# Optimization experiments

Hardware: AMD Instinct MI355X
Metric: run time of the kernel (lower is better)

Reference implementation:

```python
import jax, jax.numpy as jnp
import numpy as np

N_NODES = 100000
N_EDGES = 1600000
N_PAIRS = 500000
NFEAT = 128
NHID = 128


def _uniform(key, shape, stdv):
    return jax.random.uniform(key, shape, jnp.float32, -stdv, stdv)


def setup_inputs() -> dict:
    key = jax.random.key(0)
    ks = jax.random.split(key, 24)
    inp = {
        'x': jax.random.normal(ks[0], (N_NODES, NFEAT), jnp.float32),
        'edge_row': jax.random.randint(ks[1], (N_EDGES,), 0, N_NODES, jnp.int32),
        'edge_col': jax.random.randint(ks[2], (N_EDGES,), 0, N_NODES, jnp.int32),
        'edge_w': jax.random.uniform(ks[3], (N_EDGES,), jnp.float32),
        'x_idx': jax.random.randint(ks[4], (N_PAIRS,), 0, N_NODES, jnp.int32),
        'y_idx': jax.random.randint(ks[5], (N_PAIRS,), 0, N_NODES, jnp.int32),
    }
    stdv = 1.0 / np.sqrt(NHID)
    # GCN layers: (weight_self, weight_neighbor, bias)
    inp['gc1_ws'] = _uniform(ks[6], (NFEAT, NHID), stdv)
    inp['gc1_wn'] = _uniform(ks[7], (NFEAT, NHID), stdv)
    inp['gc1_b'] = _uniform(ks[8], (NHID,), stdv)
    inp['gc2_ws'] = _uniform(ks[9], (NHID, NHID), stdv)
    inp['gc2_wn'] = _uniform(ks[10], (NHID, NHID), stdv)
    inp['gc2_b'] = _uniform(ks[11], (NHID,), stdv)
    inp['gc3_ws'] = _uniform(ks[12], (NHID, NHID), stdv)
    inp['gc3_wn'] = _uniform(ks[13], (NHID, NHID), stdv)
    inp['gc3_b'] = _uniform(ks[14], (NHID,), stdv)
    # MLP decoder: fc1 (2*nhid -> nhid), fc2 (nhid -> 1)
    s1 = 1.0 / np.sqrt(2 * NHID)
    inp['dec_w1'] = _uniform(ks[15], (2 * NHID, NHID), s1)
    inp['dec_b1'] = _uniform(ks[16], (NHID,), s1)
    s2 = 1.0 / np.sqrt(NHID)
    inp['dec_w2'] = _uniform(ks[17], (NHID, 1), s2)
    inp['dec_b2'] = _uniform(ks[18], (1,), s2)
    return inp


def _gcn(h, ws, wn, b, row, col, w, n_nodes):
    # act_self = h @ W_self ; act_neighbor = adj @ (h @ W_neighbor)
    act_self = h @ ws
    support = h @ wn  # [N, out]
    act_nb = jax.ops.segment_sum(support[col] * w[:, None], row,
                                 num_segments=n_nodes)
    return act_self + act_nb + b


def reference(x, edge_row, edge_col, edge_w, x_idx, y_idx,
              gc1_ws, gc1_wn, gc1_b, gc2_ws, gc2_wn, gc2_b,
              gc3_ws, gc3_wn, gc3_b, dec_w1, dec_b1, dec_w2, dec_b2):
    n = x.shape[0]
    h = jax.nn.relu(_gcn(x, gc1_ws, gc1_wn, gc1_b, edge_row, edge_col, edge_w, n))
    h = jax.nn.relu(_gcn(h, gc2_ws, gc2_wn, gc2_b, edge_row, edge_col, edge_w, n))
    z = _gcn(h, gc3_ws, gc3_wn, gc3_b, edge_row, edge_col, edge_w, n)
    # edge MLP decoder on gathered node pairs
    pair = jnp.concatenate([z[x_idx], z[y_idx]], axis=1)  # [P, 2*nhid]
    hdec = jax.nn.relu(pair @ dec_w1 + dec_b1)
    p = jax.nn.sigmoid(hdec @ dec_w2 + dec_b2)  # [P, 1]
    return (p, z)
```

## Files before the change

kernel.cpp:

```cpp
#include <hip/hip_runtime.h>
#include <hip/hip_bf16.h>

#define N_NODES 100000
#define N_EDGES 1600000
#define N_PAIRS 500000
#define MPAD    100032
#define NF      128

typedef __bf16 bf16x8 __attribute__((ext_vector_type(8)));
typedef float  f32x4  __attribute__((ext_vector_type(4)));
typedef unsigned int   u32;
typedef unsigned short u16;

__device__ inline u16   f2b(float f) { __bf16 b = (__bf16)f; return __builtin_bit_cast(u16, b); }
__device__ inline float b2f(u16 u)   { return (float)__builtin_bit_cast(__bf16, u); }

__global__ void k_convT(const float* __restrict__ src, u16* __restrict__ dst, int K, int N) {
    int i = blockIdx.x * 256 + threadIdx.x;
    if (i >= K * N) return;
    int n = i / K, k = i - n * K;
    dst[i] = f2b(src[k * N + n]);
}

__global__ void k_convX(const float2* __restrict__ x, u32* __restrict__ xb) {
    int i = blockIdx.x * 256 + threadIdx.x;
    if (i >= MPAD * 64) return;
    int node = i >> 6;
    float2 v = make_float2(0.f, 0.f);
    if (node < N_NODES) v = x[i];
    xb[i] = (u32)f2b(v.x) | ((u32)f2b(v.y) << 16);
}

__global__ void k_hist(const int* __restrict__ row, int* __restrict__ deg) {
    int e = blockIdx.x * 256 + threadIdx.x;
    if (e >= N_EDGES) return;
    atomicAdd(&deg[row[e]], 1);
}

__global__ void k_scan1(const int* __restrict__ deg, int* __restrict__ incl, int* __restrict__ bsums) {
    __shared__ int s[1024];
    int t = threadIdx.x;
    int g = blockIdx.x * 1024 + t;
    s[t] = (g < N_NODES) ? deg[g] : 0;
    __syncthreads();
    for (int d = 1; d < 1024; d <<= 1) {
        int add = (t >= d) ? s[t - d] : 0;
        __syncthreads();
        s[t] += add;
        __syncthreads();
    }
    if (g < N_NODES) incl[g] = s[t];
    if (t == 1023) bsums[blockIdx.x] = s[1023];
}

__global__ void k_scan2(int* __restrict__ bsums, int nb) {
    __shared__ int s[128];
    int t = threadIdx.x;
    s[t] = (t < nb) ? bsums[t] : 0;
    __syncthreads();
    for (int d = 1; d < 128; d <<= 1) {
        int add = (t >= d) ? s[t - d] : 0;
        __syncthreads();
        s[t] += add;
        __syncthreads();
    }
    if (t < nb) bsums[t] = (t == 0) ? 0 : s[t - 1];
}

__global__ void k_scan3(const int* __restrict__ incl, const int* __restrict__ bsums,
                        int* __restrict__ rowptr, int* __restrict__ cursor) {
    int g = blockIdx.x * 256 + threadIdx.x;
    if (g == 0) { rowptr[0] = 0; cursor[0] = 0; }
    if (g >= N_NODES) return;
    int v = incl[g] + bsums[g >> 10];
    rowptr[g + 1] = v;
    if (g + 1 < N_NODES) cursor[g + 1] = v;
}

__global__ void k_scatter(const int* __restrict__ row, const int* __restrict__ col,
                          const float* __restrict__ w, int* __restrict__ cursor,
                          int* __restrict__ ccol, float* __restrict__ cw) {
    int e = blockIdx.x * 256 + threadIdx.x;
    if (e >= N_EDGES) return;
    int pos = atomicAdd(&cursor[row[e]], 1);
    ccol[pos] = col[e];
    cw[pos]   = w[e];
}

__global__ void k_gemm_pair(const u16* __restrict__ A, const u16* __restrict__ WsT,
                            const u16* __restrict__ WnT, float* __restrict__ HS,
                            u16* __restrict__ SUPc) {
    int wid = threadIdx.x >> 6, lane = threadIdx.x & 63;
    int lr = lane & 15, lg = lane >> 4;
    int m0 = blockIdx.x * 64;
    const u16* WT = (wid < 2) ? WsT : WnT;
    int n0 = (wid & 1) * 64;
    f32x4 acc[4][4] = {};
    for (int ks = 0; ks < 4; ++ks) {
        int k0 = ks * 32 + lg * 8;
        bf16x8 a[4], b[4];
        #pragma unroll
        for (int r = 0; r < 4; ++r)
            a[r] = *reinterpret_cast<const bf16x8*>(A + (size_t)(m0 + r * 16 + lr) * NF + k0);
        #pragma unroll
        for (int c = 0; c < 4; ++c)
            b[c] = *reinterpret_cast<const bf16x8*>(WT + (size_t)(n0 + c * 16 + lr) * NF + k0);
        #pragma unroll
        for (int r = 0; r < 4; ++r)
            #pragma unroll
            for (int c = 0; c < 4; ++c)
                acc[r][c] = __builtin_amdgcn_mfma_f32_16x16x32_bf16(a[r], b[c], acc[r][c], 0, 0, 0);
    }
    #pragma unroll
    for (int r = 0; r < 4; ++r) {
        #pragma unroll
        for (int reg = 0; reg < 4; ++reg) {
            int m = m0 + r * 16 + lg * 4 + reg;
            if (m >= N_NODES) continue;
            #pragma unroll
            for (int c = 0; c < 4; ++c) {
                int col = n0 + c * 16 + lr;
                float v = acc[r][c][reg];
                if (wid < 2) HS[(size_t)m * NF + col] = v;
                else {
                    int ch = col >> 4, cc = col & 15;
                    SUPc[((size_t)ch * MPAD + m) * 16 + cc] = f2b(v);
                }
            }
        }
    }
}

__global__ void k_gemm_uv(const u16* __restrict__ A, const u16* __restrict__ W1aT,
                          const u16* __restrict__ W1bT, const float* __restrict__ b1,
                          u16* __restrict__ U, u16* __restrict__ V) {
    int wid = threadIdx.x >> 6, lane = threadIdx.x & 63;
    int lr = lane & 15, lg = lane >> 4;
    int m0 = blockIdx.x * 64;
    const u16* WT = (wid < 2) ? W1aT : W1bT;
    u16* OUT = (wid < 2) ? U : V;
    int addb = (wid < 2) ? 1 : 0;
    int n0 = (wid & 1) * 64;
    f32x4 acc[4][4] = {};
    for (int ks = 0; ks < 4; ++ks) {
        int k0 = ks * 32 + lg * 8;
        bf16x8 a[4], b[4];
        #pragma unroll
        for (int r = 0; r < 4; ++r)
            a[r] = *reinterpret_cast<const bf16x8*>(A + (size_t)(m0 + r * 16 + lr) * NF + k0);
        #pragma unroll
        for (int c = 0; c < 4; ++c)
            b[c] = *reinterpret_cast<const bf16x8*>(WT + (size_t)(n0 + c * 16 + lr) * NF + k0);
        #pragma unroll
        for (int r = 0; r < 4; ++r)
            #pragma unroll
            for (int c = 0; c < 4; ++c)
                acc[r][c] = __builtin_amdgcn_mfma_f32_16x16x32_bf16(a[r], b[c], acc[r][c], 0, 0, 0);
    }
    #pragma unroll
    for (int r = 0; r < 4; ++r) {
        #pragma unroll
        for (int reg = 0; reg < 4; ++reg) {
            int m = m0 + r * 16 + lg * 4 + reg;
            #pragma unroll
            for (int c = 0; c < 4; ++c) {
                int col = n0 + c * 16 + lr;
                float v = acc[r][c][reg];
                if (addb) v += b1[col];
                OUT[(size_t)m * NF + col] = f2b(v);
            }
        }
    }
}

__global__ void k_aggregate_c(const u32* __restrict__ SUPc, const float2* __restrict__ HS2,
                              const int* __restrict__ rowptr, const int* __restrict__ ccol,
                              const float* __restrict__ cw, const float2* __restrict__ bias2,
                              u32* __restrict__ Hout, float2* __restrict__ Zout, int relu) {
    int chunk = blockIdx.x & 7;
    int nb = blockIdx.x >> 3;
    int l = threadIdx.x & 63, w = threadIdx.x >> 6;
    int sub = l >> 3, sl = l & 7;
    int node = nb * 32 + w * 8 + sub;
    if (node >= N_NODES) return;
    const u32* base = SUPc + (size_t)chunk * MPAD * 8;
    int e0 = rowptr[node], e1 = rowptr[node + 1];
    float a0 = 0.f, a1 = 0.f;
    int e = e0;
    for (; e + 4 <= e1; e += 4) {
        int c0 = ccol[e], c1 = ccol[e + 1], c2 = ccol[e + 2], c3 = ccol[e + 3];
        float w0 = cw[e], w1 = cw[e + 1], w2 = cw[e + 2], w3 = cw[e + 3];
        u32 v0 = base[(size_t)c0 * 8 + sl];
        u32 v1 = base[(size_t)c1 * 8 + sl];
        u32 v2 = base[(size_t)c2 * 8 + sl];
        u32 v3 = base[(size_t)c3 * 8 + sl];
        a0 = fmaf(w0, b2f((u16)(v0 & 0xffff)), a0); a1 = fmaf(w0, b2f((u16)(v0 >> 16)), a1);
        a0 = fmaf(w1, b2f((u16)(v1 & 0xffff)), a0); a1 = fmaf(w1, b2f((u16)(v1 >> 16)), a1);
        a0 = fmaf(w2, b2f((u16)(v2 & 0xffff)), a0); a1 = fmaf(w2, b2f((u16)(v2 >> 16)), a1);
        a0 = fmaf(w3, b2f((u16)(v3 & 0xffff)), a0); a1 = fmaf(w3, b2f((u16)(v3 >> 16)), a1);
    }
    for (; e < e1; ++e) {
        int c = ccol[e];
        float wgt = cw[e];
        u32 v = base[(size_t)c * 8 + sl];
        a0 = fmaf(wgt, b2f((u16)(v & 0xffff)), a0);
        a1 = fmaf(wgt, b2f((u16)(v >> 16)), a1);
    }
    size_t oidx = (size_t)node * 64 + chunk * 8 + sl;
    float2 hsv = HS2[oidx];
    float2 bv  = bias2[chunk * 8 + sl];
    float o0 = hsv.x + a0 + bv.x;
    float o1 = hsv.y + a1 + bv.y;
    if (relu) { o0 = fmaxf(o0, 0.f); o1 = fmaxf(o1, 0.f); }
    Hout[oidx] = (u32)f2b(o0) | ((u32)f2b(o1) << 16);
    if (Zout) Zout[oidx] = make_float2(o0, o1);
}

__global__ void k_pairdec(const u16* __restrict__ U, const u16* __restrict__ V,
                          const int* __restrict__ xidx, const int* __restrict__ yidx,
                          const float* __restrict__ w2, const float* __restrict__ b2,
                          float* __restrict__ outp) {
    int t = blockIdx.x * 256 + threadIdx.x;
    int pair = t >> 2;
    int j = t & 3;
    if (pair >= N_PAIRS) return;
    int xi = xidx[pair], yi = yidx[pair];
    const bf16x8* up = reinterpret_cast<const bf16x8*>(U + (size_t)xi * NF + j * 32);
    const bf16x8* vp = reinterpret_cast<const bf16x8*>(V + (size_t)yi * NF + j * 32);
    bf16x8 uu[4], vv[4];
    #pragma unroll
    for (int it = 0; it < 4; ++it) { uu[it] = up[it]; vv[it] = vp[it]; }
    const float4* w4 = reinterpret_cast<const float4*>(w2 + j * 32);
    float acc = 0.f;
    #pragma unroll
    for (int it = 0; it < 4; ++it) {
        float4 wa = w4[it * 2], wb = w4[it * 2 + 1];
        float h;
        h = fmaxf((float)uu[it][0] + (float)vv[it][0], 0.f); acc = fmaf(h, wa.x, acc);
        h = fmaxf((float)uu[it][1] + (float)vv[it][1], 0.f); acc = fmaf(h, wa.y, acc);
        h = fmaxf((float)uu[it][2] + (float)vv[it][2], 0.f); acc = fmaf(h, wa.z, acc);
        h = fmaxf((float)uu[it][3] + (float)vv[it][3], 0.f); acc = fmaf(h, wa.w, acc);
        h = fmaxf((float)uu[it][4] + (float)vv[it][4], 0.f); acc = fmaf(h, wb.x, acc);
        h = fmaxf((float)uu[it][5] + (float)vv[it][5], 0.f); acc = fmaf(h, wb.y, acc);
        h = fmaxf((float)uu[it][6] + (float)vv[it][6], 0.f); acc = fmaf(h, wb.z, acc);
        h = fmaxf((float)uu[it][7] + (float)vv[it][7], 0.f); acc = fmaf(h, wb.w, acc);
    }
    acc += __shfl_xor(acc, 1, 64);
    acc += __shfl_xor(acc, 2, 64);
    if (j == 0) outp[pair] = 1.f / (1.f + __expf(-(acc + b2[0])));
}

extern "C" void kernel_launch(void* const* d_in, const int* in_sizes, int n_in,
                              void* d_out, int out_size, void* d_ws, size_t ws_size,
                              hipStream_t stream) {
    const float* x      = (const float*)d_in[0];
    const int* edge_row = (const int*)d_in[1];
    const int* edge_col = (const int*)d_in[2];
    const float* edge_w = (const float*)d_in[3];
    const int* x_idx    = (const int*)d_in[4];
    const int* y_idx    = (const int*)d_in[5];
    const float* gws[3] = {(const float*)d_in[6], (const float*)d_in[9],  (const float*)d_in[12]};
    const float* gwn[3] = {(const float*)d_in[7], (const float*)d_in[10], (const float*)d_in[13]};
    const float* gb[3]  = {(const float*)d_in[8], (const float*)d_in[11], (const float*)d_in[14]};
    const float* dw1 = (const float*)d_in[15];
    const float* db1 = (const float*)d_in[16];
    const float* dw2 = (const float*)d_in[17];
    const float* db2 = (const float*)d_in[18];
    float* out_p = (float*)d_out;
    float* out_z = out_p + N_PAIRS;

    char* base = (char*)d_ws;
    size_t off = 0;
    auto alloc = [&](size_t bytes) -> void* {
        void* p = base + off;
        off = (off + bytes + 255) & ~(size_t)255;
        return p;
    };
    u16* h0   = (u16*)alloc((size_t)MPAD * NF * 2);
    u16* h1   = (u16*)alloc((size_t)MPAD * NF * 2);
    u16* supc = (u16*)alloc((size_t)MPAD * NF * 2);
    float* hs = (float*)alloc((size_t)MPAD * NF * 4);
    u16* wT[6];
    for (int i = 0; i < 6; ++i) wT[i] = (u16*)alloc(128 * 128 * 2);
    u16* w1aT = (u16*)alloc(128 * 128 * 2);
    u16* w1bT = (u16*)alloc(128 * 128 * 2);
    int* deg    = (int*)alloc(N_NODES * 4);
    int* incl   = (int*)alloc(N_NODES * 4);
    int* bsums  = (int*)alloc(128 * 4);
    int* rowptr = (int*)alloc((N_NODES + 1) * 4);
    int* cursor = (int*)alloc(N_NODES * 4);
    int* ccol   = (int*)alloc(N_EDGES * 4);
    float* cwt  = (float*)alloc(N_EDGES * 4);
    u16* U = (u16*)hs;
    u16* V = U + (size_t)MPAD * NF;

    hipMemsetAsync(deg, 0, N_NODES * 4, stream);

    for (int l = 0; l < 3; ++l) {
        k_convT<<<64, 256, 0, stream>>>(gws[l], wT[2 * l],     128, 128);
        k_convT<<<64, 256, 0, stream>>>(gwn[l], wT[2 * l + 1], 128, 128);
    }
    k_convT<<<64, 256, 0, stream>>>(dw1,             w1aT, 128, 128);
    k_convT<<<64, 256, 0, stream>>>(dw1 + 128 * 128, w1bT, 128, 128);
    k_convX<<<(MPAD * 64 + 255) / 256, 256, 0, stream>>>((const float2*)x, (u32*)h0);

    k_hist<<<(N_EDGES + 255) / 256, 256, 0, stream>>>(edge_row, deg);
    k_scan1<<<98, 1024, 0, stream>>>(deg, incl, bsums);
    k_scan2<<<1, 128, 0, stream>>>(bsums, 98);
    k_scan3<<<(N_NODES + 255) / 256, 256, 0, stream>>>(incl, bsums, rowptr, cursor);
    k_scatter<<<(N_EDGES + 255) / 256, 256, 0, stream>>>(edge_row, edge_col, edge_w, cursor, ccol, cwt);

    const int GB = MPAD / 64;
    const int AB = 8 * ((N_NODES + 31) / 32);

    k_gemm_pair<<<GB, 256, 0, stream>>>(h0, wT[0], wT[1], hs, supc);
    k_aggregate_c<<<AB, 256, 0, stream>>>((const u32*)supc, (const float2*)hs, rowptr, ccol, cwt,
                                          (const float2*)gb[0], (u32*)h1, nullptr, 1);
    k_gemm_pair<<<GB, 256, 0, stream>>>(h1, wT[2], wT[3], hs, supc);
    k_aggregate_c<<<AB, 256, 0, stream>>>((const u32*)supc, (const float2*)hs, rowptr, ccol, cwt,
                                          (const float2*)gb[1], (u32*)h0, nullptr, 1);
    k_gemm_pair<<<GB, 256, 0, stream>>>(h0, wT[4], wT[5], hs, supc);
    k_aggregate_c<<<AB, 256, 0, stream>>>((const u32*)supc, (const float2*)hs, rowptr, ccol, cwt,
                                          (const float2*)gb[2], (u32*)h1, (float2*)out_z, 0);
    k_gemm_uv<<<GB, 256, 0, stream>>>(h1, w1aT, w1bT, db1, U, V);
    k_pairdec<<<(N_PAIRS * 4 + 255) / 256, 256, 0, stream>>>(U, V, x_idx, y_idx, dw2, db2, out_p);
}
```

Measured before the change: 905.0 us.

## Pack CSR col/weight into u64, store self-activation in bf16, add nontemporal hints

The CSR column index and edge weight are packed into a single 64-bit entry, so the aggregation fetches one 8-byte value per edge instead of two separate 4-byte arrays, and the edge loop is unrolled to 8 to keep more gathers in flight. The self-term output of the paired GEMM is now stored as bf16 instead of fp32, halving its write and read traffic. Nontemporal loads and stores are added on streaming accesses to reduce cache pollution. Keeping the self-term in bf16 adds rounding error to the output z.

```diff
diff --git a/kernel.cpp b/kernel.cpp
--- a/kernel.cpp
+++ b/kernel.cpp
@@ -9,8 +9,10 @@
 
 typedef __bf16 bf16x8 __attribute__((ext_vector_type(8)));
 typedef float  f32x4  __attribute__((ext_vector_type(4)));
-typedef unsigned int   u32;
-typedef unsigned short u16;
+typedef float  f32x2  __attribute__((ext_vector_type(2)));
+typedef unsigned int       u32;
+typedef unsigned short     u16;
+typedef unsigned long long u64;
 
 __device__ inline u16   f2b(float f) { __bf16 b = (__bf16)f; return __builtin_bit_cast(u16, b); }
 __device__ inline float b2f(u16 u)   { return (float)__builtin_bit_cast(__bf16, u); }
@@ -22,12 +24,12 @@
     dst[i] = f2b(src[k * N + n]);
 }
 
-__global__ void k_convX(const float2* __restrict__ x, u32* __restrict__ xb) {
+__global__ void k_convX(const f32x2* __restrict__ x, u32* __restrict__ xb) {
     int i = blockIdx.x * 256 + threadIdx.x;
     if (i >= MPAD * 64) return;
     int node = i >> 6;
-    float2 v = make_float2(0.f, 0.f);
-    if (node < N_NODES) v = x[i];
+    f32x2 v = {0.f, 0.f};
+    if (node < N_NODES) v = __builtin_nontemporal_load(x + i);
     xb[i] = (u32)f2b(v.x) | ((u32)f2b(v.y) << 16);
 }
 
@@ -79,16 +81,18 @@
 
 __global__ void k_scatter(const int* __restrict__ row, const int* __restrict__ col,
                           const float* __restrict__ w, int* __restrict__ cursor,
-                          int* __restrict__ ccol, float* __restrict__ cw) {
+                          u64* __restrict__ cce) {
     int e = blockIdx.x * 256 + threadIdx.x;
     if (e >= N_EDGES) return;
-    int pos = atomicAdd(&cursor[row[e]], 1);
-    ccol[pos] = col[e];
-    cw[pos]   = w[e];
+    int r = __builtin_nontemporal_load(row + e);
+    int c = __builtin_nontemporal_load(col + e);
+    float wv = __builtin_nontemporal_load(w + e);
+    int pos = atomicAdd(&cursor[r], 1);
+    cce[pos] = ((u64)__builtin_bit_cast(u32, wv) << 32) | (u32)c;
 }
 
 __global__ void k_gemm_pair(const u16* __restrict__ A, const u16* __restrict__ WsT,
-                            const u16* __restrict__ WnT, float* __restrict__ HS,
+                            const u16* __restrict__ WnT, u16* __restrict__ HSb,
                             u16* __restrict__ SUPc) {
     int wid = threadIdx.x >> 6, lane = threadIdx.x & 63;
     int lr = lane & 15, lg = lane >> 4;
@@ -120,11 +124,11 @@
             #pragma unroll
             for (int c = 0; c < 4; ++c) {
                 int col = n0 + c * 16 + lr;
-                float v = acc[r][c][reg];
-                if (wid < 2) HS[(size_t)m * NF + col] = v;
+                u16 v = f2b(acc[r][c][reg]);
+                if (wid < 2) __builtin_nontemporal_store(v, HSb + (size_t)m * NF + col);
                 else {
                     int ch = col >> 4, cc = col & 15;
-                    SUPc[((size_t)ch * MPAD + m) * 16 + cc] = f2b(v);
+                    SUPc[((size_t)ch * MPAD + m) * 16 + cc] = v;
                 }
             }
         }
@@ -173,10 +177,10 @@
     }
 }
 
-__global__ void k_aggregate_c(const u32* __restrict__ SUPc, const float2* __restrict__ HS2,
-                              const int* __restrict__ rowptr, const int* __restrict__ ccol,
-                              const float* __restrict__ cw, const float2* __restrict__ bias2,
-                              u32* __restrict__ Hout, float2* __restrict__ Zout, int relu) {
+__global__ void k_aggregate_c(const u32* __restrict__ SUPc, const u32* __restrict__ HSb,
+                              const int* __restrict__ rowptr, const u64* __restrict__ cce,
+                              const f32x2* __restrict__ bias2,
+                              u32* __restrict__ Hout, f32x2* __restrict__ Zout, int relu) {
     int chunk = blockIdx.x & 7;
     int nb = blockIdx.x >> 3;
     int l = threadIdx.x & 63, w = threadIdx.x >> 6;
@@ -187,33 +191,38 @@
     int e0 = rowptr[node], e1 = rowptr[node + 1];
     float a0 = 0.f, a1 = 0.f;
     int e = e0;
-    for (; e + 4 <= e1; e += 4) {
-        int c0 = ccol[e], c1 = ccol[e + 1], c2 = ccol[e + 2], c3 = ccol[e + 3];
-        float w0 = cw[e], w1 = cw[e + 1], w2 = cw[e + 2], w3 = cw[e + 3];
-        u32 v0 = base[(size_t)c0 * 8 + sl];
-        u32 v1 = base[(size_t)c1 * 8 + sl];
-        u32 v2 = base[(size_t)c2 * 8 + sl];
-        u32 v3 = base[(size_t)c3 * 8 + sl];
-        a0 = fmaf(w0, b2f((u16)(v0 & 0xffff)), a0); a1 = fmaf(w0, b2f((u16)(v0 >> 16)), a1);
-        a0 = fmaf(w1, b2f((u16)(v1 & 0xffff)), a0); a1 = fmaf(w1, b2f((u16)(v1 >> 16)), a1);
-        a0 = fmaf(w2, b2f((u16)(v2 & 0xffff)), a0); a1 = fmaf(w2, b2f((u16)(v2 >> 16)), a1);
-        a0 = fmaf(w3, b2f((u16)(v3 & 0xffff)), a0); a1 = fmaf(w3, b2f((u16)(v3 >> 16)), a1);
+    for (; e + 8 <= e1; e += 8) {
+        u64 r[8];
+        u32 v[8];
+        #pragma unroll
+        for (int i = 0; i < 8; ++i) r[i] = __builtin_nontemporal_load(cce + e + i);
+        #pragma unroll
+        for (int i = 0; i < 8; ++i) v[i] = base[(size_t)(u32)r[i] * 8 + sl];
+        #pragma unroll
+        for (int i = 0; i < 8; ++i) {
+            float wt = __builtin_bit_cast(float, (u32)(r[i] >> 32));
+            a0 = fmaf(wt, b2f((u16)(v[i] & 0xffff)), a0);
+            a1 = fmaf(wt, b2f((u16)(v[i] >> 16)), a1);
+        }
     }
     for (; e < e1; ++e) {
-        int c = ccol[e];
-        float wgt = cw[e];
-        u32 v = base[(size_t)c * 8 + sl];
-        a0 = fmaf(wgt, b2f((u16)(v & 0xffff)), a0);
-        a1 = fmaf(wgt, b2f((u16)(v >> 16)), a1);
+        u64 rr = __builtin_nontemporal_load(cce + e);
+        u32 v = base[(size_t)(u32)rr * 8 + sl];
+        float wt = __builtin_bit_cast(float, (u32)(rr >> 32));
+        a0 = fmaf(wt, b2f((u16)(v & 0xffff)), a0);
+        a1 = fmaf(wt, b2f((u16)(v >> 16)), a1);
     }
     size_t oidx = (size_t)node * 64 + chunk * 8 + sl;
-    float2 hsv = HS2[oidx];
-    float2 bv  = bias2[chunk * 8 + sl];
-    float o0 = hsv.x + a0 + bv.x;
-    float o1 = hsv.y + a1 + bv.y;
+    u32 hsv = __builtin_nontemporal_load(HSb + oidx);
+    f32x2 bv = bias2[chunk * 8 + sl];
+    float o0 = b2f((u16)(hsv & 0xffff)) + a0 + bv.x;
+    float o1 = b2f((u16)(hsv >> 16)) + a1 + bv.y;
     if (relu) { o0 = fmaxf(o0, 0.f); o1 = fmaxf(o1, 0.f); }
-    Hout[oidx] = (u32)f2b(o0) | ((u32)f2b(o1) << 16);
-    if (Zout) Zout[oidx] = make_float2(o0, o1);
+    __builtin_nontemporal_store((u32)f2b(o0) | ((u32)f2b(o1) << 16), Hout + oidx);
+    if (Zout) {
+        f32x2 z = {o0, o1};
+        __builtin_nontemporal_store(z, Zout + oidx);
+    }
 }
 
 __global__ void k_pairdec(const u16* __restrict__ U, const u16* __restrict__ V,
@@ -224,7 +233,8 @@
     int pair = t >> 2;
     int j = t & 3;
     if (pair >= N_PAIRS) return;
-    int xi = xidx[pair], yi = yidx[pair];
+    int xi = __builtin_nontemporal_load(xidx + pair);
+    int yi = __builtin_nontemporal_load(yidx + pair);
     const bf16x8* up = reinterpret_cast<const bf16x8*>(U + (size_t)xi * NF + j * 32);
     const bf16x8* vp = reinterpret_cast<const bf16x8*>(V + (size_t)yi * NF + j * 32);
     bf16x8 uu[4], vv[4];
@@ -279,7 +289,7 @@
     u16* h0   = (u16*)alloc((size_t)MPAD * NF * 2);
     u16* h1   = (u16*)alloc((size_t)MPAD * NF * 2);
     u16* supc = (u16*)alloc((size_t)MPAD * NF * 2);
-    float* hs = (float*)alloc((size_t)MPAD * NF * 4);
+    u16* hsb  = (u16*)alloc((size_t)MPAD * NF * 4);
     u16* wT[6];
     for (int i = 0; i < 6; ++i) wT[i] = (u16*)alloc(128 * 128 * 2);
     u16* w1aT = (u16*)alloc(128 * 128 * 2);
@@ -289,12 +299,11 @@
     int* bsums  = (int*)alloc(128 * 4);
     int* rowptr = (int*)alloc((N_NODES + 1) * 4);
     int* cursor = (int*)alloc(N_NODES * 4);
-    int* ccol   = (int*)alloc(N_EDGES * 4);
-    float* cwt  = (float*)alloc(N_EDGES * 4);
-    u16* U = (u16*)hs;
+    u64* cce    = (u64*)alloc((size_t)N_EDGES * 8);
+    u16* U = hsb;
     u16* V = U + (size_t)MPAD * NF;
 
-    hipMemsetAsync(deg, 0, N_NODES * 4, stream);
+    (void)hipMemsetAsync(deg, 0, N_NODES * 4, stream);
 
     for (int l = 0; l < 3; ++l) {
         k_convT<<<64, 256, 0, stream>>>(gws[l], wT[2 * l],     128, 128);
@@ -302,26 +311,26 @@
     }
     k_convT<<<64, 256, 0, stream>>>(dw1,             w1aT, 128, 128);
     k_convT<<<64, 256, 0, stream>>>(dw1 + 128 * 128, w1bT, 128, 128);
-    k_convX<<<(MPAD * 64 + 255) / 256, 256, 0, stream>>>((const float2*)x, (u32*)h0);
+    k_convX<<<(MPAD * 64 + 255) / 256, 256, 0, stream>>>((const f32x2*)x, (u32*)h0);
 
     k_hist<<<(N_EDGES + 255) / 256, 256, 0, stream>>>(edge_row, deg);
     k_scan1<<<98, 1024, 0, stream>>>(deg, incl, bsums);
     k_scan2<<<1, 128, 0, stream>>>(bsums, 98);
     k_scan3<<<(N_NODES + 255) / 256, 256, 0, stream>>>(incl, bsums, rowptr, cursor);
-    k_scatter<<<(N_EDGES + 255) / 256, 256, 0, stream>>>(edge_row, edge_col, edge_w, cursor, ccol, cwt);
+    k_scatter<<<(N_EDGES + 255) / 256, 256, 0, stream>>>(edge_row, edge_col, edge_w, cursor, cce);
 
     const int GB = MPAD / 64;
     const int AB = 8 * ((N_NODES + 31) / 32);
 
-    k_gemm_pair<<<GB, 256, 0, stream>>>(h0, wT[0], wT[1], hs, supc);
-    k_aggregate_c<<<AB, 256, 0, stream>>>((const u32*)supc, (const float2*)hs, rowptr, ccol, cwt,
-                                          (const float2*)gb[0], (u32*)h1, nullptr, 1);
-    k_gemm_pair<<<GB, 256, 0, stream>>>(h1, wT[2], wT[3], hs, supc);
-    k_aggregate_c<<<AB, 256, 0, stream>>>((const u32*)supc, (const float2*)hs, rowptr, ccol, cwt,
-                                          (const float2*)gb[1], (u32*)h0, nullptr, 1);
-    k_gemm_pair<<<GB, 256, 0, stream>>>(h0, wT[4], wT[5], hs, supc);
-    k_aggregate_c<<<AB, 256, 0, stream>>>((const u32*)supc, (const float2*)hs, rowptr, ccol, cwt,
-                                          (const float2*)gb[2], (u32*)h1, (float2*)out_z, 0);
+    k_gemm_pair<<<GB, 256, 0, stream>>>(h0, wT[0], wT[1], hsb, supc);
+    k_aggregate_c<<<AB, 256, 0, stream>>>((const u32*)supc, (const u32*)hsb, rowptr, cce,
+                                          (const f32x2*)gb[0], (u32*)h1, nullptr, 1);
+    k_gemm_pair<<<GB, 256, 0, stream>>>(h1, wT[2], wT[3], hsb, supc);
+    k_aggregate_c<<<AB, 256, 0, stream>>>((const u32*)supc, (const u32*)hsb, rowptr, cce,
+                                          (const f32x2*)gb[1], (u32*)h0, nullptr, 1);
+    k_gemm_pair<<<GB, 256, 0, stream>>>(h0, wT[4], wT[5], hsb, supc);
+    k_aggregate_c<<<AB, 256, 0, stream>>>((const u32*)supc, (const u32*)hsb, rowptr, cce,
+                                          (const f32x2*)gb[2], (u32*)h1, (f32x2*)out_z, 0);
     k_gemm_uv<<<GB, 256, 0, stream>>>(h1, w1aT, w1bT, db1, U, V);
     k_pairdec<<<(N_PAIRS * 4 + 255) / 256, 256, 0, stream>>>(U, V, x_idx, y_idx, dw2, db2, out_p);
 }
```

New measurement: 1.245 ms. 37.6% more time.
